# Optimization experiments

Hardware: AMD Instinct MI355X
Metric: run time of the kernel (lower is better)

The kernel has to match this reference:

```python
import jax, jax.numpy as jnp
import numpy as np

PROB_THRESHOLD = 0.5  # default prob_threshold from the torch forward signature


def setup_inputs() -> dict:
    key = jax.random.key(0)
    mask = jax.random.uniform(key, (64, 512, 896), dtype=jnp.float32)  # per-pixel probabilities
    return {"mask": mask, "n_pts_threshold": 10, "dist_threshold": 64}


def rag_forward(mask, n_pts_threshold, dist_threshold, prob_threshold=PROB_THRESHOLD):
    # mask: [B, H, W] probability map.
    B, H, W = mask.shape
    binary = mask > prob_threshold                      # [B, H, W]
    n_pts = jnp.sum(binary, axis=(1, 2))                # [B] count of foreground points
    rows_any = jnp.any(binary, axis=2)                  # [B, H]
    cols_any = jnp.any(binary, axis=1)                  # [B, W]
    ridx = jnp.arange(H)
    cidx = jnp.arange(W)
    # Bounding box of foreground points (sentinels make empty rows/cols harmless).
    rmin = jnp.min(jnp.where(rows_any, ridx[None, :], H), axis=1)
    rmax = jnp.max(jnp.where(rows_any, ridx[None, :], -1), axis=1)
    cmin = jnp.min(jnp.where(cols_any, cidx[None, :], W), axis=1)
    cmax = jnp.max(jnp.where(cols_any, cidx[None, :], -1), axis=1)
    # Dilate box by dist_threshold and clip to image bounds.
    rmin = jnp.maximum(rmin - dist_threshold, 0)
    rmax = jnp.minimum(rmax + dist_threshold, H - 1)
    cmin = jnp.maximum(cmin - dist_threshold, 0)
    cmax = jnp.minimum(cmax + dist_threshold, W - 1)
    row_in = (ridx[None, :] >= rmin[:, None]) & (ridx[None, :] <= rmax[:, None])  # [B, H]
    col_in = (cidx[None, :] >= cmin[:, None]) & (cidx[None, :] <= cmax[:, None])  # [B, W]
    in_box = row_in[:, :, None] & col_in[:, None, :]                              # [B, H, W]
    # Too few confident points -> attend everywhere (all-ones map).
    enough = (n_pts >= n_pts_threshold)[:, None, None]
    att = jnp.where(enough, in_box, True).astype(mask.dtype)
    return att


def reference(mask, n_pts_threshold, dist_threshold):
    return rag_forward(mask, n_pts_threshold, dist_threshold)
```

## Files before the change

### kernel.cpp

```cpp
#include <hip/hip_runtime.h>

#define B 64
#define H 512
#define W 896
#define W4 (W / 4)
#define PIX_PER_BATCH (H * W)
#define VEC_PER_BATCH (PIX_PER_BATCH / 4)
#define TPB 256
#define VEC_PER_THREAD 8
#define VEC_PER_BLOCK (TPB * VEC_PER_THREAD)
#define BLOCKS_PER_BATCH (VEC_PER_BATCH / VEC_PER_BLOCK)
#define PROB_THRESHOLD 0.5f

struct BoxWs {
    int cnt[B];
    int rmn[B];
    int rmx[B];
    int cmn[B];
    int cmx[B];
};

__global__ void rag_init_kernel(BoxWs* __restrict__ ws) {
    int i = threadIdx.x;
    if (i < B) {
        ws->cnt[i] = 0;
        ws->rmn[i] = H;
        ws->rmx[i] = -1;
        ws->cmn[i] = W;
        ws->cmx[i] = -1;
    }
}

__global__ __launch_bounds__(TPB) void rag_reduce_kernel(
        const float* __restrict__ mask, BoxWs* __restrict__ ws) {
    const int b = blockIdx.y;
    const float4* m = reinterpret_cast<const float4*>(mask + (size_t)b * PIX_PER_BATCH);
    const int base = blockIdx.x * VEC_PER_BLOCK + threadIdx.x;

    int cnt = 0;
    int rmn = H, rmx = -1, cmn = W, cmx = -1;

#pragma unroll
    for (int it = 0; it < VEC_PER_THREAD; ++it) {
        const int i4 = base + it * TPB;
        const float4 v = m[i4];
        const int row = i4 / W4;
        const int col = (i4 - row * W4) * 4;
        const bool f0 = v.x > PROB_THRESHOLD;
        const bool f1 = v.y > PROB_THRESHOLD;
        const bool f2 = v.z > PROB_THRESHOLD;
        const bool f3 = v.w > PROB_THRESHOLD;
        cnt += (int)f0 + (int)f1 + (int)f2 + (int)f3;
        if (f0 | f1 | f2 | f3) {
            rmn = min(rmn, row);
            rmx = max(rmx, row);
            const int clo = f0 ? col : (f1 ? col + 1 : (f2 ? col + 2 : col + 3));
            const int chi = f3 ? col + 3 : (f2 ? col + 2 : (f1 ? col + 1 : col));
            cmn = min(cmn, clo);
            cmx = max(cmx, chi);
        }
    }

#pragma unroll
    for (int off = 32; off > 0; off >>= 1) {
        cnt += __shfl_down(cnt, off);
        rmn = min(rmn, __shfl_down(rmn, off));
        rmx = max(rmx, __shfl_down(rmx, off));
        cmn = min(cmn, __shfl_down(cmn, off));
        cmx = max(cmx, __shfl_down(cmx, off));
    }

    __shared__ int s[5][TPB / 64];
    const int wave = threadIdx.x >> 6;
    if ((threadIdx.x & 63) == 0) {
        s[0][wave] = cnt;
        s[1][wave] = rmn;
        s[2][wave] = rmx;
        s[3][wave] = cmn;
        s[4][wave] = cmx;
    }
    __syncthreads();
    if (threadIdx.x == 0) {
#pragma unroll
        for (int wv = 1; wv < TPB / 64; ++wv) {
            cnt += s[0][wv];
            rmn = min(rmn, s[1][wv]);
            rmx = max(rmx, s[2][wv]);
            cmn = min(cmn, s[3][wv]);
            cmx = max(cmx, s[4][wv]);
        }
        atomicAdd(&ws->cnt[b], cnt);
        atomicMin(&ws->rmn[b], rmn);
        atomicMax(&ws->rmx[b], rmx);
        atomicMin(&ws->cmn[b], cmn);
        atomicMax(&ws->cmx[b], cmx);
    }
}

__global__ __launch_bounds__(TPB) void rag_fill_kernel(
        const BoxWs* __restrict__ ws,
        const int* __restrict__ nthr_p,
        const int* __restrict__ dthr_p,
        float* __restrict__ out) {
    const int b = blockIdx.y;
    const int nthr = *nthr_p;
    const int dthr = *dthr_p;

    const bool enough = ws->cnt[b] >= nthr;
    const int rmn = max(ws->rmn[b] - dthr, 0);
    const int rmx = min(ws->rmx[b] + dthr, H - 1);
    const int cmn = max(ws->cmn[b] - dthr, 0);
    const int cmx = min(ws->cmx[b] + dthr, W - 1);

    float4* o = reinterpret_cast<float4*>(out + (size_t)b * PIX_PER_BATCH);
    const int base = blockIdx.x * VEC_PER_BLOCK + threadIdx.x;

#pragma unroll
    for (int it = 0; it < VEC_PER_THREAD; ++it) {
        const int i4 = base + it * TPB;
        const int row = i4 / W4;
        const int col = (i4 - row * W4) * 4;
        const bool rin = (row >= rmn) & (row <= rmx);
        float4 v;
        v.x = (!enough || (rin & (col + 0 >= cmn) & (col + 0 <= cmx))) ? 1.0f : 0.0f;
        v.y = (!enough || (rin & (col + 1 >= cmn) & (col + 1 <= cmx))) ? 1.0f : 0.0f;
        v.z = (!enough || (rin & (col + 2 >= cmn) & (col + 2 <= cmx))) ? 1.0f : 0.0f;
        v.w = (!enough || (rin & (col + 3 >= cmn) & (col + 3 <= cmx))) ? 1.0f : 0.0f;
        o[i4] = v;
    }
}

extern "C" void kernel_launch(void* const* d_in, const int* in_sizes, int n_in,
                              void* d_out, int out_size, void* d_ws, size_t ws_size,
                              hipStream_t stream) {
    const float* mask  = (const float*)d_in[0];
    const int*   nthr  = (const int*)d_in[1];
    const int*   dthr  = (const int*)d_in[2];
    float*       out   = (float*)d_out;
    BoxWs*       ws    = (BoxWs*)d_ws;

    rag_init_kernel<<<1, 256, 0, stream>>>(ws);

    dim3 grid(BLOCKS_PER_BATCH, B);
    rag_reduce_kernel<<<grid, TPB, 0, stream>>>(mask, ws);
    rag_fill_kernel<<<grid, TPB, 0, stream>>>(ws, nthr, dthr, out);
}
```

Before: 216.9 us.

## Replace atomic box reduction with per-block partials and drop init kernel

The init kernel and the global atomics are removed. Each reduce block now writes its own partial count and box to a slot in the workspace, and each fill block re-reduces the 32 partials for its batch with wave shuffles before filling. This saves one launch and avoids atomic contention. The grid changes from 56 blocks of 8 iterations per batch to 32 blocks of 14 iterations, so there are fewer blocks. Row and column index math in the reduce loop now runs only when a foreground pixel is found.

```diff
diff --git a/kernel.cpp b/kernel.cpp
--- a/kernel.cpp
+++ b/kernel.cpp
@@ -4,54 +4,39 @@
 #define H 512
 #define W 896
 #define W4 (W / 4)
-#define PIX_PER_BATCH (H * W)
-#define VEC_PER_BATCH (PIX_PER_BATCH / 4)
+#define PIX (H * W)
+#define VEC (PIX / 4)
 #define TPB 256
-#define VEC_PER_THREAD 8
-#define VEC_PER_BLOCK (TPB * VEC_PER_THREAD)
-#define BLOCKS_PER_BATCH (VEC_PER_BATCH / VEC_PER_BLOCK)
-#define PROB_THRESHOLD 0.5f
+#define SLICES 32
+#define VEC_SLICE (VEC / SLICES)
+#define ITERS (VEC_SLICE / TPB)
+#define NBLK (B * SLICES)
+#define PT 0.5f
 
-struct BoxWs {
-    int cnt[B];
-    int rmn[B];
-    int rmx[B];
-    int cmn[B];
-    int cmx[B];
-};
-
-__global__ void rag_init_kernel(BoxWs* __restrict__ ws) {
-    int i = threadIdx.x;
-    if (i < B) {
-        ws->cnt[i] = 0;
-        ws->rmn[i] = H;
-        ws->rmx[i] = -1;
-        ws->cmn[i] = W;
-        ws->cmx[i] = -1;
-    }
-}
 
 __global__ __launch_bounds__(TPB) void rag_reduce_kernel(
-        const float* __restrict__ mask, BoxWs* __restrict__ ws) {
-    const int b = blockIdx.y;
-    const float4* m = reinterpret_cast<const float4*>(mask + (size_t)b * PIX_PER_BATCH);
-    const int base = blockIdx.x * VEC_PER_BLOCK + threadIdx.x;
+        const float* __restrict__ mask, int* __restrict__ ws) {
+    const int bid = blockIdx.x;
+    const int b   = bid >> 5;
+    const int tid = threadIdx.x;
+    const int sbase = (bid & (SLICES - 1)) * VEC_SLICE + tid;
 
-    int cnt = 0;
-    int rmn = H, rmx = -1, cmn = W, cmx = -1;
+    const float4* m = reinterpret_cast<const float4*>(mask) + (size_t)b * VEC;
+
+    int cnt = 0, rmn = H, rmx = -1, cmn = W, cmx = -1;
 
 #pragma unroll
-    for (int it = 0; it < VEC_PER_THREAD; ++it) {
-        const int i4 = base + it * TPB;
+    for (int it = 0; it < ITERS; ++it) {
+        const int i4 = sbase + it * TPB;
         const float4 v = m[i4];
-        const int row = i4 / W4;
-        const int col = (i4 - row * W4) * 4;
-        const bool f0 = v.x > PROB_THRESHOLD;
-        const bool f1 = v.y > PROB_THRESHOLD;
-        const bool f2 = v.z > PROB_THRESHOLD;
-        const bool f3 = v.w > PROB_THRESHOLD;
+        const bool f0 = v.x > PT;
+        const bool f1 = v.y > PT;
+        const bool f2 = v.z > PT;
+        const bool f3 = v.w > PT;
         cnt += (int)f0 + (int)f1 + (int)f2 + (int)f3;
         if (f0 | f1 | f2 | f3) {
+            const int row = i4 / W4;
+            const int col = (i4 - row * W4) * 4;
             rmn = min(rmn, row);
             rmx = max(rmx, row);
             const int clo = f0 ? col : (f1 ? col + 1 : (f2 ? col + 2 : col + 3));
@@ -71,16 +56,13 @@
     }
 
     __shared__ int s[5][TPB / 64];
-    const int wave = threadIdx.x >> 6;
-    if ((threadIdx.x & 63) == 0) {
-        s[0][wave] = cnt;
-        s[1][wave] = rmn;
-        s[2][wave] = rmx;
-        s[3][wave] = cmn;
-        s[4][wave] = cmx;
+    const int wave = tid >> 6;
+    if ((tid & 63) == 0) {
+        s[0][wave] = cnt; s[1][wave] = rmn; s[2][wave] = rmx;
+        s[3][wave] = cmn; s[4][wave] = cmx;
     }
     __syncthreads();
-    if (threadIdx.x == 0) {
+    if (tid == 0) {
 #pragma unroll
         for (int wv = 1; wv < TPB / 64; ++wv) {
             cnt += s[0][wv];
@@ -89,59 +71,84 @@
             cmn = min(cmn, s[3][wv]);
             cmx = max(cmx, s[4][wv]);
         }
-        atomicAdd(&ws->cnt[b], cnt);
-        atomicMin(&ws->rmn[b], rmn);
-        atomicMax(&ws->rmx[b], rmx);
-        atomicMin(&ws->cmn[b], cmn);
-        atomicMax(&ws->cmx[b], cmx);
+        ws[0 * NBLK + bid] = cnt;
+        ws[1 * NBLK + bid] = rmn;
+        ws[2 * NBLK + bid] = rmx;
+        ws[3 * NBLK + bid] = cmn;
+        ws[4 * NBLK + bid] = cmx;
     }
 }
 
 __global__ __launch_bounds__(TPB) void rag_fill_kernel(
-        const BoxWs* __restrict__ ws,
+        const int* __restrict__ ws,
         const int* __restrict__ nthr_p,
         const int* __restrict__ dthr_p,
         float* __restrict__ out) {
-    const int b = blockIdx.y;
-    const int nthr = *nthr_p;
-    const int dthr = *dthr_p;
+    const int bid = blockIdx.x;
+    const int b   = bid >> 5;
+    const int tid = threadIdx.x;
 
-    const bool enough = ws->cnt[b] >= nthr;
-    const int rmn = max(ws->rmn[b] - dthr, 0);
-    const int rmx = min(ws->rmx[b] + dthr, H - 1);
-    const int cmn = max(ws->cmn[b] - dthr, 0);
-    const int cmx = min(ws->cmx[b] + dthr, W - 1);
+    __shared__ int sbox[4];
+    if (tid < 64) {
+        const int q = (b << 5) + (tid & 31);
+        int c  = ws[0 * NBLK + q];
+        int r0 = ws[1 * NBLK + q];
+        int r1 = ws[2 * NBLK + q];
+        int c0 = ws[3 * NBLK + q];
+        int c1 = ws[4 * NBLK + q];
+#pragma unroll
+        for (int off = 16; off > 0; off >>= 1) {
+            c  += __shfl_xor(c, off, 32);
+            r0 = min(r0, __shfl_xor(r0, off, 32));
+            r1 = max(r1, __shfl_xor(r1, off, 32));
+            c0 = min(c0, __shfl_xor(c0, off, 32));
+            c1 = max(c1, __shfl_xor(c1, off, 32));
+        }
+        if (tid == 0) {
+            const int nthr = *nthr_p;
+            const int dthr = *dthr_p;
+            int brmn, brmx, bcmn, bcmx;
+            if (c >= nthr) {
+                brmn = max(r0 - dthr, 0);
+                brmx = min(r1 + dthr, H - 1);
+                bcmn = max(c0 - dthr, 0);
+                bcmx = min(c1 + dthr, W - 1);
+            } else {
+                brmn = 0; brmx = H - 1; bcmn = 0; bcmx = W - 1;
+            }
+            sbox[0] = brmn; sbox[1] = brmx; sbox[2] = bcmn; sbox[3] = bcmx;
+        }
+    }
+    __syncthreads();
+    const int brmn = sbox[0], brmx = sbox[1], bcmn = sbox[2], bcmx = sbox[3];
 
-    float4* o = reinterpret_cast<float4*>(out + (size_t)b * PIX_PER_BATCH);
-    const int base = blockIdx.x * VEC_PER_BLOCK + threadIdx.x;
+    float4* ob = reinterpret_cast<float4*>(out) + (size_t)b * VEC;
+    const int sbase = (bid & (SLICES - 1)) * VEC_SLICE + tid;
 
 #pragma unroll
-    for (int it = 0; it < VEC_PER_THREAD; ++it) {
-        const int i4 = base + it * TPB;
+    for (int it = 0; it < ITERS; ++it) {
+        const int i4 = sbase + it * TPB;
         const int row = i4 / W4;
         const int col = (i4 - row * W4) * 4;
-        const bool rin = (row >= rmn) & (row <= rmx);
+        const bool rin = (row >= brmn) & (row <= brmx);
         float4 v;
-        v.x = (!enough || (rin & (col + 0 >= cmn) & (col + 0 <= cmx))) ? 1.0f : 0.0f;
-        v.y = (!enough || (rin & (col + 1 >= cmn) & (col + 1 <= cmx))) ? 1.0f : 0.0f;
-        v.z = (!enough || (rin & (col + 2 >= cmn) & (col + 2 <= cmx))) ? 1.0f : 0.0f;
-        v.w = (!enough || (rin & (col + 3 >= cmn) & (col + 3 <= cmx))) ? 1.0f : 0.0f;
-        o[i4] = v;
+        v.x = (rin & (col + 0 >= bcmn) & (col + 0 <= bcmx)) ? 1.0f : 0.0f;
+        v.y = (rin & (col + 1 >= bcmn) & (col + 1 <= bcmx)) ? 1.0f : 0.0f;
+        v.z = (rin & (col + 2 >= bcmn) & (col + 2 <= bcmx)) ? 1.0f : 0.0f;
+        v.w = (rin & (col + 3 >= bcmn) & (col + 3 <= bcmx)) ? 1.0f : 0.0f;
+        ob[i4] = v;
     }
 }
 
 extern "C" void kernel_launch(void* const* d_in, const int* in_sizes, int n_in,
                               void* d_out, int out_size, void* d_ws, size_t ws_size,
                               hipStream_t stream) {
-    const float* mask  = (const float*)d_in[0];
-    const int*   nthr  = (const int*)d_in[1];
-    const int*   dthr  = (const int*)d_in[2];
-    float*       out   = (float*)d_out;
-    BoxWs*       ws    = (BoxWs*)d_ws;
+    const float* mask = (const float*)d_in[0];
+    const int*   nthr = (const int*)d_in[1];
+    const int*   dthr = (const int*)d_in[2];
+    float*       out  = (float*)d_out;
+    int*         ws   = (int*)d_ws;
 
-    rag_init_kernel<<<1, 256, 0, stream>>>(ws);
-
-    dim3 grid(BLOCKS_PER_BATCH, B);
-    rag_reduce_kernel<<<grid, TPB, 0, stream>>>(mask, ws);
-    rag_fill_kernel<<<grid, TPB, 0, stream>>>(ws, nthr, dthr, out);
+    rag_reduce_kernel<<<NBLK, TPB, 0, stream>>>(mask, ws);
+    rag_fill_kernel<<<NBLK, TPB, 0, stream>>>(ws, nthr, dthr, out);
 }
```

Measured after the change: 211.4 us. 2.6% less time.
